# Kernel tuning notes

Hardware: AMD Instinct MI355X
Metric: run time of the kernel (lower is better)

## Reference

```python
import jax, jax.numpy as jnp
import numpy as np

_EPS = 1e-5
RC = 5.0   # cutoff radius
L = 20     # number of radial basis functions
N = 10000  # nodes
E = 100000 # edges
F = 128    # in_feats


def _ssp(x):
    # ShiftedSoftplus: softplus(x) - log(2)
    return jax.nn.softplus(x) - jnp.log(2.0)


def _rbf(r):
    # DimeNet radial basis: sqrt(2/rc) * sin(n*pi*r/rc) / r, n = 1..L.  r: [E,1] -> [E,L]
    n = jnp.arange(1, L + 1, dtype=r.dtype)
    return jnp.sqrt(2.0 / RC) * jnp.sin(n * jnp.pi * r / RC) / r


def _fc(u):
    # cosine cutoff applied elementwise: 0.5*(cos(pi*u/rc)+1) for u < rc else 0
    return jnp.where(u < RC, 0.5 * (jnp.cos(jnp.pi * u / RC) + 1.0), 0.0)


def setup_inputs() -> dict:
    key = jax.random.key(0)
    ks = jax.random.split(key, 12)

    def nrm(k, shape, scale=1.0):
        return jax.random.normal(k, shape, dtype=jnp.float32) * scale

    return {
        "x": nrm(ks[0], (N, 3)) * 3.0,           # atomic positions
        "v": nrm(ks[1], (N, F, 3)),               # vector node features
        "s": nrm(ks[2], (N, F)),                  # scalar node features
        "ms1_w": nrm(ks[3], (F, F), F ** -0.5),
        "ms1_b": jnp.zeros((F,), jnp.float32),
        "ms2_w": nrm(ks[4], (3 * F, F), F ** -0.5),
        "ms2_b": jnp.zeros((3 * F,), jnp.float32),
        "mv_w": nrm(ks[5], (3 * F, L), L ** -0.5),
        "mv_b": jnp.zeros((3 * F,), jnp.float32),
        "us1_w": nrm(ks[6], (F, F), F ** -0.5),
        "us1_b": jnp.zeros((F,), jnp.float32),
        "us2_w": nrm(ks[7], (3 * F, F), F ** -0.5),
        "us2_b": jnp.zeros((3 * F,), jnp.float32),
        "src": jax.random.randint(ks[8], (E,), 0, N, dtype=jnp.int32),
        "dst": jax.random.randint(ks[9], (E,), 0, N, dtype=jnp.int32),
    }


def reference(x, v, s, ms1_w, ms1_b, ms2_w, ms2_b, mv_w, mv_b,
              us1_w, us1_b, us2_w, us2_b, src, dst):
    # ---------- pass 1: message1 + reduce1 (sum over incoming edges) ----------
    sj = s[src]                                   # [E,F]   src scalar features
    vj = v[src]                                   # [E,F,3] src vector features
    vec = x[src] - x[dst]                         # [E,3]   x_i - x_j (molecule branch)
    r = jnp.sqrt(jnp.sum(vec ** 2, axis=-1) + _EPS)[:, None]          # [E,1]
    phi = _ssp(sj @ ms1_w.T + ms1_b) @ ms2_w.T + ms2_b                 # [E,3F]
    w = _fc(_rbf(r) @ mv_w.T + mv_b)                                    # [E,3F]
    v_, s_, r_ = jnp.split(phi * w, 3, axis=-1)                         # each [E,F]
    dv_e = vj * v_[:, :, None] + r_[:, :, None] * (vec / r)[:, None, :] # [E,F,3]
    dv = jax.ops.segment_sum(dv_e, dst, num_segments=N)                 # [N,F,3]
    ds = jax.ops.segment_sum(s_, dst, num_segments=N)                   # [N,F]
    v_new = v + dv
    s_new = s + ds

    # ---------- pass 2: message2 + reduce2 (mean over incoming edges) ----------
    s2 = _ssp(s_new[src] @ us1_w.T + us1_b) @ us2_w.T + us2_b           # [E,3F]
    deg = jax.ops.segment_sum(jnp.ones((E,), s.dtype), dst, num_segments=N)
    denom = jnp.maximum(deg, 1.0)
    s_mean = jax.ops.segment_sum(s2, dst, num_segments=N) / denom[:, None]        # [N,3F]
    uv = jax.ops.segment_sum(v_new[src], dst, num_segments=N) / denom[:, None, None]  # [N,F,3]
    avv, asv, ass = jnp.split(s_mean, 3, axis=-1)                       # each [N,F]
    norm = jnp.sqrt(jnp.sum(uv ** 2, axis=-1) + _EPS)[..., None]        # [N,F,1]
    dv2 = uv * avv[:, :, None]                                           # [N,F,3]
    ds2 = jnp.sum((uv / norm) ** 2, axis=-1) * asv + ass                 # [N,F]
    return (v_new + dv2, s_new + ds2)
```

## Files before the change

### kernel.cpp

```cpp
#include <hip/hip_runtime.h>
#include <hip/hip_bf16.h>


#define F_DIM   128
#define F3_DIM  384
#define L_DIM   20
#define CAP     64
#define BATCH   16

typedef __attribute__((ext_vector_type(8))) short short8;
typedef __attribute__((ext_vector_type(4))) float f32x4;
typedef __attribute__((ext_vector_type(4))) unsigned short us4;

struct u3 { unsigned a, b, c; };

__device__ __forceinline__ unsigned short f2bf(float f) {
  union { float f; unsigned u; } a; a.f = f;
  unsigned u = a.u;
  u = (u + 0x7FFFu + ((u >> 16) & 1u)) >> 16;
  return (unsigned short)u;
}
__device__ __forceinline__ float bf2f(unsigned short u) {
  union { unsigned u; float f; } a; a.u = ((unsigned)u) << 16;
  return a.f;
}

__global__ __launch_bounds__(256) void cast_fill_kernel(
    const float* __restrict__ ms1_w, unsigned short* __restrict__ w_ms1,
    const float* __restrict__ ms2_w, unsigned short* __restrict__ w_ms2,
    const float* __restrict__ us1_w, unsigned short* __restrict__ w_us1,
    const float* __restrict__ us2_w, unsigned short* __restrict__ w_us2,
    const float* __restrict__ s,     unsigned short* __restrict__ sbf,
    const float* __restrict__ mv_w,  unsigned short* __restrict__ mvwB,
    const int* __restrict__ src, const int* __restrict__ dst,
    int* __restrict__ cursor, int* __restrict__ jbuf,
    unsigned short* __restrict__ c1pad, unsigned short* __restrict__ v4pad,
    int nF, int E)
{
  int i = blockIdx.x * 256 + threadIdx.x;
  if (i < 16384) w_ms1[i] = f2bf(ms1_w[i]);
  if (i < 49152) w_ms2[i] = f2bf(ms2_w[i]);
  if (i < 16384) w_us1[i] = f2bf(us1_w[i]);
  if (i < 49152) w_us2[i] = f2bf(us2_w[i]);
  if (i < nF)    sbf[i] = f2bf(s[i]);
  if (i < 384 * 32) {
    int o = i >> 5, k = i & 31;
    float val = (k < 20) ? mv_w[o * 20 + k] * 0.6324555320336759f : 0.f;
    mvwB[i] = f2bf(val);
  }
  if (i < 768) c1pad[i] = 0;
  if (i < 512) v4pad[i] = 0;
  if (i < E) {
    int d = dst[i];
    int p = atomicAdd(&cursor[d], 1);
    if (p < CAP) jbuf[d * CAP + p] = src[i];
  }
}

__global__ __launch_bounds__(512) void mlp_kernel(
    const unsigned short* __restrict__ X,
    const unsigned short* __restrict__ W1,
    const float* __restrict__ B1,
    const unsigned short* __restrict__ W2,
    const float* __restrict__ B2,
    const float* __restrict__ Vfp,
    unsigned short* __restrict__ Yc)
{
  __shared__ float HT[128 * 17];
  const int lane = threadIdx.x & 63;
  const int wave = threadIdx.x >> 6;
  const int c    = lane & 15;
  const int quad = lane >> 4;
  const int m0   = blockIdx.x * 16;

  f32x4 acc = (f32x4){0.f, 0.f, 0.f, 0.f};
#pragma unroll
  for (int kk = 0; kk < 4; kk++) {
    short8 a = *(const short8*)(X + (size_t)(m0 + c) * 128 + kk * 32 + quad * 8);
    short8 b = *(const short8*)(W1 + (size_t)(wave * 16 + c) * 128 + kk * 32 + quad * 8);
    acc = __builtin_amdgcn_mfma_f32_16x16x32_bf16(a, b, acc, 0, 0, 0);
  }
  {
    int k = wave * 16 + c;
    float bias = B1[k];
#pragma unroll
    for (int r = 0; r < 4; r++) {
      float h = acc[r] + bias;
      float sp = (h > 15.f) ? h : log1pf(__expf(h));
      sp -= 0.69314718056f;
      HT[k * 17 + quad * 4 + r] = sp;
    }
  }
  __syncthreads();

  f32x4 acc2[3];
#pragma unroll
  for (int g = 0; g < 3; g++) acc2[g] = (f32x4){0.f, 0.f, 0.f, 0.f};
#pragma unroll
  for (int kk = 0; kk < 4; kk++) {
    short8 afr;
#pragma unroll
    for (int j = 0; j < 8; j++) {
      float hv = HT[(kk * 32 + quad * 8 + j) * 17 + c];
      afr[j] = (short)f2bf(hv);
    }
#pragma unroll
    for (int g = 0; g < 3; g++) {
      short8 b = *(const short8*)(W2 + (size_t)(g * 128 + wave * 16 + c) * 128 + kk * 32 + quad * 8);
      acc2[g] = __builtin_amdgcn_mfma_f32_16x16x32_bf16(afr, b, acc2[g], 0, 0, 0);
    }
  }
  {
    int f = wave * 16 + c;
    float b0 = B2[f], b1 = B2[128 + f], b2 = B2[256 + f];
#pragma unroll
    for (int r = 0; r < 4; r++) {
      int m = quad * 4 + r;
      const float* vp = Vfp + ((size_t)(m0 + m) * 128 + f) * 3;
      unsigned p0 = f2bf(acc2[0][r] + b0);
      unsigned p1 = f2bf(acc2[1][r] + b1);
      unsigned p2 = f2bf(acc2[2][r] + b2);
      u3 rec;
      rec.a = p0 | (p1 << 16);
      rec.b = p2 | ((unsigned)f2bf(vp[0]) << 16);
      rec.c = (unsigned)f2bf(vp[1]) | ((unsigned)f2bf(vp[2]) << 16);
      *(u3*)(Yc + ((size_t)(m0 + m) * 128 + f) * 6) = rec;
    }
  }
}

__global__ __launch_bounds__(512) void hidden_kernel(
    const unsigned short* __restrict__ X,
    const unsigned short* __restrict__ W1,
    const float* __restrict__ B1,
    us4* __restrict__ V4)
{
  const int lane = threadIdx.x & 63;
  const int wave = threadIdx.x >> 6;
  const int c    = lane & 15;
  const int quad = lane >> 4;
  const int m0   = blockIdx.x * 16;

  f32x4 acc = (f32x4){0.f, 0.f, 0.f, 0.f};
#pragma unroll
  for (int kk = 0; kk < 4; kk++) {
    short8 a = *(const short8*)(X + (size_t)(m0 + c) * 128 + kk * 32 + quad * 8);
    short8 b = *(const short8*)(W1 + (size_t)(wave * 16 + c) * 128 + kk * 32 + quad * 8);
    acc = __builtin_amdgcn_mfma_f32_16x16x32_bf16(a, b, acc, 0, 0, 0);
  }
  int f = wave * 16 + c;
  float bias = B1[f];
#pragma unroll
  for (int r = 0; r < 4; r++) {
    int m = m0 + quad * 4 + r;
    float h = acc[r] + bias;
    float sp = (h > 15.f) ? h : log1pf(__expf(h));
    sp -= 0.69314718056f;
    us4 rec = V4[(size_t)m * 128 + f];
    rec.w = f2bf(sp);
    V4[(size_t)m * 128 + f] = rec;
  }
}

__global__ __launch_bounds__(256, 4) void pass1_kernel(
    const float* __restrict__ x,
    const unsigned short* __restrict__ combo1,
    const float* __restrict__ v,
    const float* __restrict__ s,
    const unsigned short* __restrict__ mvwB,
    const float* __restrict__ mv_b,
    const int* __restrict__ jbuf,
    const int* __restrict__ deg,
    float* __restrict__ vnew, us4* __restrict__ vnew4,
    float* __restrict__ snew, unsigned short* __restrict__ snew_bf, int nNodes)
{
  __shared__ unsigned short Asn[BATCH * 32];
  __shared__ float4 Au[BATCH];
  __shared__ us4 Wl[BATCH * 128];
  __shared__ float red[512];

  const int tid  = threadIdx.x;
  const int wave = tid >> 6, lane = tid & 63;
  const int half = wave >> 1, split = wave & 1;
  const int i = blockIdx.x;
  const int f = lane + 64 * half;
  const int c = lane & 15, quad = lane >> 4;

  int cnt = deg[i]; if (cnt > CAP) cnt = CAP;
  const int base = i * CAP;

  short8 bfr[6]; float bias[6];
#pragma unroll
  for (int p = 0; p < 3; p++)
#pragma unroll
    for (int h = 0; h < 2; h++) {
      int t = 2 * wave + h + 8 * p;
      bfr[p * 2 + h]  = *(const short8*)(mvwB + (size_t)(t * 16 + c) * 32 + quad * 8);
      bias[p * 2 + h] = mv_b[t * 16 + c];
    }

  const float xi0 = x[i * 3], xi1 = x[i * 3 + 1], xi2 = x[i * 3 + 2];
  int jv = (lane < cnt) ? jbuf[base + lane] : nNodes;

  float accV0 = 0.f, accV1 = 0.f, accV2 = 0.f, accS = 0.f;

  for (int bs = 0; bs < cnt; bs += BATCH) {
    int bcnt = cnt - bs; if (bcnt > BATCH) bcnt = BATCH;
    __syncthreads();

    {
      int e  = tid >> 4;
      int li = tid & 15;
      int j  = __shfl(jv, bs + e);
      if (e < bcnt) {
        float d0 = x[j * 3]     - xi0;
        float d1 = x[j * 3 + 1] - xi1;
        float d2 = x[j * 3 + 2] - xi2;
        float r = sqrtf(d0 * d0 + d1 * d1 + d2 * d2 + 1e-5f);
        float invr = 1.0f / r;
        if (li == 0) Au[e] = make_float4(d0 * invr, d1 * invr, d2 * invr, invr);
        float theta = r * 0.6283185307179586f;
        Asn[e * 32 + li] = f2bf(__sinf((float)(li + 1) * theta));
        unsigned short hiv = 0;
        if (li < 4) hiv = f2bf(__sinf((float)(li + 17) * theta));
        Asn[e * 32 + 16 + li] = hiv;
      }
    }
    __syncthreads();

    {
      short8 a = *(const short8*)&Asn[c * 32 + quad * 8];
      f32x4 acc[6];
#pragma unroll
      for (int q = 0; q < 6; q++)
        acc[q] = __builtin_amdgcn_mfma_f32_16x16x32_bf16(
            a, bfr[q], (f32x4){0.f, 0.f, 0.f, 0.f}, 0, 0, 0);
#pragma unroll
      for (int r = 0; r < 4; r++) {
        int el = quad * 4 + r;
        if (el < bcnt) {
          float invr = Au[el].w;
#pragma unroll
          for (int h = 0; h < 2; h++) {
            float wp0 = fmaf(acc[h][r],     invr, bias[h]);
            float wp1 = fmaf(acc[2 + h][r], invr, bias[2 + h]);
            float wp2 = fmaf(acc[4 + h][r], invr, bias[4 + h]);
            float w0 = (wp0 < 5.f) ? 0.5f * (__cosf(wp0 * 0.6283185307179586f) + 1.f) : 0.f;
            float w1 = (wp1 < 5.f) ? 0.5f * (__cosf(wp1 * 0.6283185307179586f) + 1.f) : 0.f;
            float w2 = (wp2 < 5.f) ? 0.5f * (__cosf(wp2 * 0.6283185307179586f) + 1.f) : 0.f;
            us4 o; o.x = f2bf(w0); o.y = f2bf(w1); o.z = f2bf(w2); o.w = 0;
            Wl[el * 128 + wave * 32 + h * 16 + c] = o;
          }
        }
      }
    }
    __syncthreads();

    u3 cb[8];
#pragma unroll
    for (int k = 0; k < 8; k++) {
      int j = __shfl(jv, bs + split + 2 * k);
      cb[k] = *(const u3*)(combo1 + ((size_t)j * 128 + f) * 6);
    }
#pragma unroll
    for (int k = 0; k < 8; k++) {
      int el = split + 2 * k;
      if (el < bcnt) {
        float4 u = Au[el];
        us4 wv = Wl[el * 128 + f];
        float ph0 = bf2f((unsigned short)(cb[k].a & 0xffff));
        float ph1 = bf2f((unsigned short)(cb[k].a >> 16));
        float ph2 = bf2f((unsigned short)(cb[k].b & 0xffff));
        float vx  = bf2f((unsigned short)(cb[k].b >> 16));
        float vy  = bf2f((unsigned short)(cb[k].c & 0xffff));
        float vz  = bf2f((unsigned short)(cb[k].c >> 16));
        float m0 = ph0 * bf2f(wv.x);
        float m1 = ph1 * bf2f(wv.y);
        float m2 = ph2 * bf2f(wv.z);
        accV0 = fmaf(vx, m0, fmaf(m2, u.x, accV0));
        accV1 = fmaf(vy, m0, fmaf(m2, u.y, accV1));
        accV2 = fmaf(vz, m0, fmaf(m2, u.z, accV2));
        accS += m1;
      }
    }
  }

  const int idx = half * 64 + lane;
  __syncthreads();
  if (split == 1) {
    red[idx * 4 + 0] = accV0; red[idx * 4 + 1] = accV1;
    red[idx * 4 + 2] = accV2; red[idx * 4 + 3] = accS;
  }
  __syncthreads();
  if (split == 0) {
    accV0 += red[idx * 4 + 0]; accV1 += red[idx * 4 + 1];
    accV2 += red[idx * 4 + 2]; accS  += red[idx * 4 + 3];
    size_t b3 = (size_t)i * 384 + f * 3;
    float n0 = v[b3] + accV0, n1 = v[b3 + 1] + accV1, n2 = v[b3 + 2] + accV2;
    vnew[b3] = n0; vnew[b3 + 1] = n1; vnew[b3 + 2] = n2;
    us4 o; o.x = f2bf(n0); o.y = f2bf(n1); o.z = f2bf(n2); o.w = 0;
    vnew4[(size_t)i * 128 + f] = o;
    size_t b1 = (size_t)i * 128 + f;
    float sv = s[b1] + accS;
    snew[b1] = sv;
    snew_bf[b1] = f2bf(sv);
  }
}

__global__ __launch_bounds__(512, 2) void pass2_kernel(
    const us4* __restrict__ vnew4,
    const int* __restrict__ jbuf, const int* __restrict__ deg,
    const unsigned short* __restrict__ W2,
    const float* __restrict__ B2,
    const float* __restrict__ vnew,
    const float* __restrict__ snew,
    float* __restrict__ vout, float* __restrict__ sout, int nNodes)
{
  __shared__ unsigned short HMb[16][136];
  __shared__ float UV[16 * 128 * 3];

  const int tid  = threadIdx.x;
  const int wave = tid >> 6, lane = tid & 63;
  const int c    = lane & 15, quad = lane >> 4;
  const int m0   = blockIdx.x * 16;

  const int ra = 2 * wave, rb = ra + 1;
  const int na = m0 + ra, nb = m0 + rb;
  int ca = deg[na]; if (ca > CAP) ca = CAP;
  int cb = deg[nb]; if (cb > CAP) cb = CAP;
  int jva = (lane < ca) ? jbuf[na * CAP + lane] : nNodes;
  int jvb = (lane < cb) ? jbuf[nb * CAP + lane] : nNodes;

  float a0l = 0.f, a1l = 0.f, a2l = 0.f, ahl = 0.f;
  float a0h = 0.f, a1h = 0.f, a2h = 0.f, ahh = 0.f;
  float b0l = 0.f, b1l = 0.f, b2l = 0.f, bhl = 0.f;
  float b0h = 0.f, b1h = 0.f, b2h = 0.f, bhh = 0.f;

  int emax = (ca > cb) ? ca : cb;
  for (int e = 0; e < emax; e += 4) {
    us4 ral[4], rah[4], rbl[4], rbh[4];
#pragma unroll
    for (int k = 0; k < 4; k++) {
      int ja = __shfl(jva, e + k);
      int jb = __shfl(jvb, e + k);
      ral[k] = vnew4[(size_t)ja * 128 + lane];
      rah[k] = vnew4[(size_t)ja * 128 + lane + 64];
      rbl[k] = vnew4[(size_t)jb * 128 + lane];
      rbh[k] = vnew4[(size_t)jb * 128 + lane + 64];
    }
#pragma unroll
    for (int k = 0; k < 4; k++) {
      a0l += bf2f(ral[k].x); a1l += bf2f(ral[k].y);
      a2l += bf2f(ral[k].z); ahl += bf2f(ral[k].w);
      a0h += bf2f(rah[k].x); a1h += bf2f(rah[k].y);
      a2h += bf2f(rah[k].z); ahh += bf2f(rah[k].w);
      b0l += bf2f(rbl[k].x); b1l += bf2f(rbl[k].y);
      b2l += bf2f(rbl[k].z); bhl += bf2f(rbl[k].w);
      b0h += bf2f(rbh[k].x); b1h += bf2f(rbh[k].y);
      b2h += bf2f(rbh[k].z); bhh += bf2f(rbh[k].w);
    }
  }

  float dia = 1.0f / (float)(ca > 0 ? ca : 1);
  float dib = 1.0f / (float)(cb > 0 ? cb : 1);
  {
    int fl = lane, fh = lane + 64;
    UV[(ra * 128 + fl) * 3 + 0] = a0l * dia;
    UV[(ra * 128 + fl) * 3 + 1] = a1l * dia;
    UV[(ra * 128 + fl) * 3 + 2] = a2l * dia;
    UV[(ra * 128 + fh) * 3 + 0] = a0h * dia;
    UV[(ra * 128 + fh) * 3 + 1] = a1h * dia;
    UV[(ra * 128 + fh) * 3 + 2] = a2h * dia;
    UV[(rb * 128 + fl) * 3 + 0] = b0l * dib;
    UV[(rb * 128 + fl) * 3 + 1] = b1l * dib;
    UV[(rb * 128 + fl) * 3 + 2] = b2l * dib;
    UV[(rb * 128 + fh) * 3 + 0] = b0h * dib;
    UV[(rb * 128 + fh) * 3 + 1] = b1h * dib;
    UV[(rb * 128 + fh) * 3 + 2] = b2h * dib;
    HMb[ra][fl] = f2bf(ahl * dia);
    HMb[ra][fh] = f2bf(ahh * dia);
    HMb[rb][fl] = f2bf(bhl * dib);
    HMb[rb][fh] = f2bf(bhh * dib);
  }
  __syncthreads();

  f32x4 acc2[3];
#pragma unroll
  for (int g = 0; g < 3; g++) acc2[g] = (f32x4){0.f, 0.f, 0.f, 0.f};
#pragma unroll
  for (int kk = 0; kk < 4; kk++) {
    short8 afr = *(const short8*)&HMb[c][kk * 32 + quad * 8];
#pragma unroll
    for (int g = 0; g < 3; g++) {
      short8 b = *(const short8*)(W2 + (size_t)(g * 128 + wave * 16 + c) * 128 + kk * 32 + quad * 8);
      acc2[g] = __builtin_amdgcn_mfma_f32_16x16x32_bf16(afr, b, acc2[g], 0, 0, 0);
    }
  }

  int f = wave * 16 + c;
  float bb0 = B2[f], bb1 = B2[128 + f], bb2 = B2[256 + f];
#pragma unroll
  for (int r = 0; r < 4; r++) {
    int m = quad * 4 + r;
    int gm = m0 + m;
    float z = (deg[gm] > 0) ? 1.f : 0.f;
    float avv = (acc2[0][r] + bb0) * z;
    float asv = (acc2[1][r] + bb1) * z;
    float ass = (acc2[2][r] + bb2) * z;
    float uv0 = UV[(m * 128 + f) * 3 + 0];
    float uv1 = UV[(m * 128 + f) * 3 + 1];
    float uv2 = UV[(m * 128 + f) * 3 + 2];
    float q = uv0 * uv0 + uv1 * uv1 + uv2 * uv2;
    float ds2 = (q / (q + 1e-5f)) * asv + ass;
    size_t b3 = (size_t)gm * 384 + f * 3;
    vout[b3]     = vnew[b3]     + uv0 * avv;
    vout[b3 + 1] = vnew[b3 + 1] + uv1 * avv;
    vout[b3 + 2] = vnew[b3 + 2] + uv2 * avv;
    size_t b1i = (size_t)gm * 128 + f;
    sout[b1i] = snew[b1i] + ds2;
  }
}

extern "C" void kernel_launch(void* const* d_in, const int* in_sizes, int n_in,
                              void* d_out, int out_size, void* d_ws, size_t ws_size,
                              hipStream_t stream)
{
  const float* x     = (const float*)d_in[0];
  const float* v     = (const float*)d_in[1];
  const float* s     = (const float*)d_in[2];
  const float* ms1_w = (const float*)d_in[3];
  const float* ms1_b = (const float*)d_in[4];
  const float* ms2_w = (const float*)d_in[5];
  const float* ms2_b = (const float*)d_in[6];
  const float* mv_w  = (const float*)d_in[7];
  const float* mv_b  = (const float*)d_in[8];
  const float* us1_w = (const float*)d_in[9];
  const float* us1_b = (const float*)d_in[10];
  const float* us2_w = (const float*)d_in[11];
  const float* us2_b = (const float*)d_in[12];
  const int*   src   = (const int*)d_in[13];
  const int*   dst   = (const int*)d_in[14];

  const int N = in_sizes[0] / 3;
  const int E = in_sizes[13];

  char* p = (char*)d_ws;
  auto alloc = [&](size_t bytes) -> void* {
    void* r = (void*)p;
    p += (bytes + 255) & ~(size_t)255;
    return r;
  };
  unsigned short* sbf   = (unsigned short*)alloc((size_t)N * 128 * 2);
  unsigned short* snbf  = (unsigned short*)alloc((size_t)N * 128 * 2);
  unsigned short* w_ms1 = (unsigned short*)alloc(16384 * 2);
  unsigned short* w_ms2 = (unsigned short*)alloc(49152 * 2);
  unsigned short* w_us1 = (unsigned short*)alloc(16384 * 2);
  unsigned short* w_us2 = (unsigned short*)alloc(49152 * 2);
  unsigned short* mvwB  = (unsigned short*)alloc(384 * 32 * 2);
  us4*   vnew4  = (us4*)alloc((size_t)(N + 1) * 128 * 8);
  unsigned short* combo1 = (unsigned short*)alloc((size_t)(N + 1) * 128 * 12);
  float* vnew   = (float*)alloc((size_t)N * 384 * 4);
  float* snew   = (float*)alloc((size_t)N * 128 * 4);
  int* cursor   = (int*)alloc((size_t)N * 4);
  int* jbuf     = (int*)alloc((size_t)N * CAP * 4);

  hipMemsetAsync(cursor, 0, (size_t)N * 4, stream);

  cast_fill_kernel<<<(N * 128 + 255) / 256, 256, 0, stream>>>(
      ms1_w, w_ms1, ms2_w, w_ms2, us1_w, w_us1, us2_w, w_us2,
      s, sbf, mv_w, mvwB, src, dst, cursor, jbuf,
      combo1 + (size_t)N * 768, (unsigned short*)(vnew4 + (size_t)N * 128),
      N * 128, E);

  mlp_kernel<<<N / 16, 512, 0, stream>>>(sbf, w_ms1, ms1_b, w_ms2, ms2_b,
                                         v, combo1);

  pass1_kernel<<<N, 256, 0, stream>>>(x, combo1, v, s, mvwB, mv_b,
                                      jbuf, cursor, vnew, vnew4, snew, snbf, N);

  hidden_kernel<<<N / 16, 512, 0, stream>>>(snbf, w_us1, us1_b, vnew4);

  float* vout = (float*)d_out;
  float* sout = vout + (size_t)N * 384;
  pass2_kernel<<<N / 16, 512, 0, stream>>>(vnew4, jbuf, cursor, w_us2, us2_b,
                                           vnew, snew, vout, sout, N);
}
```

Before: 209.9 us.

## Double pass1 block to 512 threads, splitting edges across four waves per feature half

The per-node pass1 kernel now launches 512 threads (8 waves) instead of 256. Each wave computes one MFMA tile of the edge-weight projection instead of two, and each feature half is split four ways over edges instead of two. A larger shared-memory reduction then combines the four partial sums. The aim is more parallelism and memory-level concurrency per node for the gather-heavy inner loop. The cost is a bigger reduction step, more shared memory, and more idle threads for low-degree nodes.

After: 245.2 us. 16.8% more time.

```diff
diff --git a/kernel.cpp b/kernel.cpp
--- a/kernel.cpp
+++ b/kernel.cpp
@@ -162,7 +162,7 @@
   }
 }
 
-__global__ __launch_bounds__(256, 4) void pass1_kernel(
+__global__ __launch_bounds__(512, 8) void pass1_kernel(
     const float* __restrict__ x,
     const unsigned short* __restrict__ combo1,
     const float* __restrict__ v,
@@ -177,11 +177,11 @@
   __shared__ unsigned short Asn[BATCH * 32];
   __shared__ float4 Au[BATCH];
   __shared__ us4 Wl[BATCH * 128];
-  __shared__ float red[512];
+  __shared__ float red[4 * 3 * 128];
 
   const int tid  = threadIdx.x;
   const int wave = tid >> 6, lane = tid & 63;
-  const int half = wave >> 1, split = wave & 1;
+  const int half = wave >> 2, split = wave & 3;
   const int i = blockIdx.x;
   const int f = lane + 64 * half;
   const int c = lane & 15, quad = lane >> 4;
@@ -189,15 +189,13 @@
   int cnt = deg[i]; if (cnt > CAP) cnt = CAP;
   const int base = i * CAP;
 
-  short8 bfr[6]; float bias[6];
-#pragma unroll
-  for (int p = 0; p < 3; p++)
-#pragma unroll
-    for (int h = 0; h < 2; h++) {
-      int t = 2 * wave + h + 8 * p;
-      bfr[p * 2 + h]  = *(const short8*)(mvwB + (size_t)(t * 16 + c) * 32 + quad * 8);
-      bias[p * 2 + h] = mv_b[t * 16 + c];
-    }
+  short8 bfr[3]; float bias[3];
+#pragma unroll
+  for (int p = 0; p < 3; p++) {
+    int t = wave + 8 * p;
+    bfr[p]  = *(const short8*)(mvwB + (size_t)(t * 16 + c) * 32 + quad * 8);
+    bias[p] = mv_b[t * 16 + c];
+  }
 
   const float xi0 = x[i * 3], xi1 = x[i * 3 + 1], xi2 = x[i * 3 + 2];
   int jv = (lane < cnt) ? jbuf[base + lane] : nNodes;
@@ -211,7 +209,8 @@
     {
       int e  = tid >> 4;
       int li = tid & 15;
-      int j  = __shfl(jv, bs + e);
+      int se = (e < BATCH) ? bs + e : 0;
+      int j  = __shfl(jv, se);
       if (e < bcnt) {
         float d0 = x[j * 3]     - xi0;
         float d1 = x[j * 3 + 1] - xi1;
@@ -230,41 +229,38 @@
 
     {
       short8 a = *(const short8*)&Asn[c * 32 + quad * 8];
-      f32x4 acc[6];
-#pragma unroll
-      for (int q = 0; q < 6; q++)
-        acc[q] = __builtin_amdgcn_mfma_f32_16x16x32_bf16(
-            a, bfr[q], (f32x4){0.f, 0.f, 0.f, 0.f}, 0, 0, 0);
+      f32x4 acc[3];
+#pragma unroll
+      for (int p = 0; p < 3; p++)
+        acc[p] = __builtin_amdgcn_mfma_f32_16x16x32_bf16(
+            a, bfr[p], (f32x4){0.f, 0.f, 0.f, 0.f}, 0, 0, 0);
 #pragma unroll
       for (int r = 0; r < 4; r++) {
         int el = quad * 4 + r;
         if (el < bcnt) {
           float invr = Au[el].w;
-#pragma unroll
-          for (int h = 0; h < 2; h++) {
-            float wp0 = fmaf(acc[h][r],     invr, bias[h]);
-            float wp1 = fmaf(acc[2 + h][r], invr, bias[2 + h]);
-            float wp2 = fmaf(acc[4 + h][r], invr, bias[4 + h]);
-            float w0 = (wp0 < 5.f) ? 0.5f * (__cosf(wp0 * 0.6283185307179586f) + 1.f) : 0.f;
-            float w1 = (wp1 < 5.f) ? 0.5f * (__cosf(wp1 * 0.6283185307179586f) + 1.f) : 0.f;
-            float w2 = (wp2 < 5.f) ? 0.5f * (__cosf(wp2 * 0.6283185307179586f) + 1.f) : 0.f;
-            us4 o; o.x = f2bf(w0); o.y = f2bf(w1); o.z = f2bf(w2); o.w = 0;
-            Wl[el * 128 + wave * 32 + h * 16 + c] = o;
-          }
+          float wp0 = fmaf(acc[0][r], invr, bias[0]);
+          float wp1 = fmaf(acc[1][r], invr, bias[1]);
+          float wp2 = fmaf(acc[2][r], invr, bias[2]);
+          float w0 = (wp0 < 5.f) ? 0.5f * (__cosf(wp0 * 0.6283185307179586f) + 1.f) : 0.f;
+          float w1 = (wp1 < 5.f) ? 0.5f * (__cosf(wp1 * 0.6283185307179586f) + 1.f) : 0.f;
+          float w2 = (wp2 < 5.f) ? 0.5f * (__cosf(wp2 * 0.6283185307179586f) + 1.f) : 0.f;
+          us4 o; o.x = f2bf(w0); o.y = f2bf(w1); o.z = f2bf(w2); o.w = 0;
+          Wl[el * 128 + wave * 16 + c] = o;
         }
       }
     }
     __syncthreads();
 
-    u3 cb[8];
-#pragma unroll
-    for (int k = 0; k < 8; k++) {
-      int j = __shfl(jv, bs + split + 2 * k);
+    u3 cb[4];
+#pragma unroll
+    for (int k = 0; k < 4; k++) {
+      int j = __shfl(jv, bs + split + 4 * k);
       cb[k] = *(const u3*)(combo1 + ((size_t)j * 128 + f) * 6);
     }
 #pragma unroll
-    for (int k = 0; k < 8; k++) {
-      int el = split + 2 * k;
+    for (int k = 0; k < 4; k++) {
+      int el = split + 4 * k;
       if (el < bcnt) {
         float4 u = Au[el];
         us4 wv = Wl[el * 128 + f];
@@ -285,16 +281,24 @@
     }
   }
 
-  const int idx = half * 64 + lane;
   __syncthreads();
-  if (split == 1) {
-    red[idx * 4 + 0] = accV0; red[idx * 4 + 1] = accV1;
-    red[idx * 4 + 2] = accV2; red[idx * 4 + 3] = accS;
+  if (split != 0) {
+    int o = (split - 1) * 128 + f;
+    red[0 * 384 + o] = accV0;
+    red[1 * 384 + o] = accV1;
+    red[2 * 384 + o] = accV2;
+    red[3 * 384 + o] = accS;
   }
   __syncthreads();
   if (split == 0) {
-    accV0 += red[idx * 4 + 0]; accV1 += red[idx * 4 + 1];
-    accV2 += red[idx * 4 + 2]; accS  += red[idx * 4 + 3];
+#pragma unroll
+    for (int q = 0; q < 3; q++) {
+      int o = q * 128 + f;
+      accV0 += red[0 * 384 + o];
+      accV1 += red[1 * 384 + o];
+      accV2 += red[2 * 384 + o];
+      accS  += red[3 * 384 + o];
+    }
     size_t b3 = (size_t)i * 384 + f * 3;
     float n0 = v[b3] + accV0, n1 = v[b3 + 1] + accV1, n2 = v[b3 + 2] + accV2;
     vnew[b3] = n0; vnew[b3 + 1] = n1; vnew[b3 + 2] = n2;
@@ -475,7 +479,7 @@
   mlp_kernel<<<N / 16, 512, 0, stream>>>(sbf, w_ms1, ms1_b, w_ms2, ms2_b,
                                          v, combo1);
 
-  pass1_kernel<<<N, 256, 0, stream>>>(x, combo1, v, s, mvwB, mv_b,
+  pass1_kernel<<<N, 512, 0, stream>>>(x, combo1, v, s, mvwB, mv_b,
                                       jbuf, cursor, vnew, vnew4, snew, snbf, N);
 
   hidden_kernel<<<N / 16, 512, 0, stream>>>(snbf, w_us1, us1_b, vnew4);
```
